# Kernel tuning notes

Hardware: AMD Instinct MI355X
Metric: run time of the kernel (lower is better)

## Reference

```python
import jax, jax.numpy as jnp
import numpy as np

N_HEAD = 16
NEG_INF = -1e9


def setup_inputs() -> dict:
    key = jax.random.key(0)
    k1, k2, k3 = jax.random.split(key, 3)
    B, S, D = 4, 1024, 1024
    x = jax.random.normal(k1, (B, S, D), dtype=jnp.float32)
    w_attn = jax.random.normal(k2, (D, 3 * D), dtype=jnp.float32) * 0.02
    b_attn = jnp.zeros((3 * D,), dtype=jnp.float32)
    w_proj = jax.random.normal(k3, (D, D), dtype=jnp.float32) * 0.02
    b_proj = jnp.zeros((D,), dtype=jnp.float32)
    return {"x": x, "w_attn": w_attn, "b_attn": b_attn,
            "w_proj": w_proj, "b_proj": b_proj}


def reference(x, w_attn, b_attn, w_proj, b_proj):
    B, S, D = x.shape
    H = N_HEAD
    hd = D // H
    # fused QKV Conv1D: addmm over flattened tokens
    qkv = x @ w_attn + b_attn                      # [B,S,3D]
    q, k, v = jnp.split(qkv, 3, axis=-1)           # each [B,S,D]
    # split heads -> [B,H,S,hd]
    def heads(t):
        return t.reshape(B, S, H, hd).transpose(0, 2, 1, 3)
    q, k, v = heads(q), heads(k), heads(v)
    # scaled dot-product with causal mask
    scores = jnp.einsum('bhqd,bhkd->bhqk', q, k) / jnp.sqrt(jnp.float32(hd))
    causal = jnp.tril(jnp.ones((S, S), dtype=bool))[None, None]  # [1,1,S,S]
    scores = jnp.where(causal, scores, NEG_INF)
    attn = jax.nn.softmax(scores, axis=-1)
    out = jnp.einsum('bhqk,bhkd->bhqd', attn, v)   # [B,H,S,hd]
    out = out.transpose(0, 2, 1, 3).reshape(B, S, D)  # merge heads
    # output projection Conv1D
    return out @ w_proj + b_proj
```

## Files before the change

### kernel.cpp

```cpp
#include <hip/hip_runtime.h>
#include <hip/hip_bf16.h>

typedef __attribute__((ext_vector_type(8))) __bf16 bf16x8;
typedef __attribute__((ext_vector_type(4))) float f32x4;

__device__ __forceinline__ unsigned short f2bf(float f) {
  unsigned int u = __builtin_bit_cast(unsigned int, f);
  u += 0x7fffu + ((u >> 16) & 1u);
  return (unsigned short)(u >> 16);
}

__device__ __forceinline__ unsigned int cvtpk_bf16(float a, float b) {
  unsigned int r;
  asm("v_cvt_pk_bf16_f32 %0, %1, %2" : "=v"(r) : "v"(a), "v"(b));
  return r;
}

__device__ __forceinline__ void gll16(const void* g, void* l) {
  __builtin_amdgcn_global_load_lds(
      (const __attribute__((address_space(1))) void*)g,
      (__attribute__((address_space(3))) void*)l, 16, 0, 0);
}

__device__ __forceinline__ bf16x8 lds_frag(const unsigned short* base, int row, int kbyte) {
  int off = row * 128 + (kbyte ^ ((row & 7) << 4));
  return *(const bf16x8*)((const char*)base + off);
}

#define QUAD(AF, BV, MO)                                                       \
  asm volatile("s_waitcnt lgkmcnt(0)" ::: "memory");                           \
  __builtin_amdgcn_sched_barrier(0);                                           \
  __builtin_amdgcn_s_setprio(1);                                               \
  _Pragma("unroll") for (int j = 0; j < 4; ++j)                                \
      _Pragma("unroll") for (int ni = 0; ni < 4; ++ni)                         \
          acc[MO + j][ni] = __builtin_amdgcn_mfma_f32_16x16x32_bf16(           \
              AF[j], BV[ni], acc[MO + j][ni], 0, 0, 0);                        \
  __builtin_amdgcn_s_setprio(0);                                               \
  __builtin_amdgcn_sched_barrier(0);

__global__ __launch_bounds__(256) void prep(
    const float* __restrict__ x, unsigned short* __restrict__ xb,
    const float* __restrict__ wa, unsigned short* __restrict__ waT,
    const float* __restrict__ wp, unsigned short* __restrict__ wpT) {
  __shared__ float tile[32][33];
  const int b = blockIdx.x;
  const int t = threadIdx.x;
  if (b < 4096) {
    int i = (b * 256 + t) * 4;
    float4 v = *(const float4*)(x + i);
    ushort4 o;
    o.x = f2bf(v.x); o.y = f2bf(v.y); o.z = f2bf(v.z); o.w = f2bf(v.w);
    *(ushort4*)(xb + i) = o;
    return;
  }
  const float* in;
  unsigned short* out;
  int bid, N;
  if (b < 7168) { in = wa; out = waT; bid = b - 4096; N = 3072; }
  else          { in = wp; out = wpT; bid = b - 7168; N = 1024; }
  const int K = 1024;
  int nb = N >> 5;
  int bx = bid % nb, by = bid / nb;
  int n0 = bx << 5, k0 = by << 5;
  int c = t & 31, r0 = t >> 5;
#pragma unroll
  for (int i = 0; i < 4; ++i) {
    int r = r0 + i * 8;
    tile[r][c] = in[(size_t)(k0 + r) * N + n0 + c];
  }
  __syncthreads();
#pragma unroll
  for (int i = 0; i < 4; ++i) {
    int r = r0 + i * 8;
    out[(size_t)(n0 + r) * K + k0 + c] = f2bf(tile[c][r]);
  }
}

__global__ __launch_bounds__(512, 2) void gemm_qkv256(
    const unsigned short* __restrict__ A, const unsigned short* __restrict__ Bt,
    const float* __restrict__ bias,
    unsigned short* __restrict__ Qg, unsigned short* __restrict__ Kg,
    unsigned short* __restrict__ Vtg, int K) {
  __shared__ __align__(16) unsigned short SMEM[65536];
  unsigned short* const A0 = SMEM;
  unsigned short* const B0 = SMEM + 16384;
  unsigned short* const A1 = SMEM + 32768;
  unsigned short* const B1 = SMEM + 49152;
  const int t = threadIdx.x;
  const int l = t & 63, lr = l & 15, hi = l >> 4;
  const int w = t >> 6;
  const int wr = w >> 2, wc = w & 3;
  const int bid = (int)(blockIdx.x % 8) * 24 + (int)(blockIdx.x / 8);
  const int bm = bid / 12, bn = bid % 12;
  const int m0 = bm << 8, n0 = bn << 8;
  const int wbase = (t & ~63) * 8;

  f32x4 acc[8][4] = {};

  auto stage_half = [&](int kt, int h, unsigned short* Ad, unsigned short* Bd) {
    const unsigned short* src;
    unsigned short* dst;
    if (h < 2) { src = A  + (size_t)(m0 + h * 128) * K + kt * 64;       dst = Ad + h * 8192; }
    else       { src = Bt + (size_t)(n0 + (h - 2) * 128) * K + kt * 64; dst = Bd + (h - 2) * 8192; }
#pragma unroll
    for (int i = 0; i < 2; ++i) {
      int ci = i * 512 + t;
      int row = ci >> 3, cpos = ci & 7;
      int c = cpos ^ (row & 7);
      gll16(src + (size_t)row * K + c * 8, dst + i * 4096 + wbase);
    }
  };

  auto lda = [&](bf16x8* af, const unsigned short* Ac, int mo, int kb) {
#pragma unroll
    for (int j = 0; j < 4; ++j)
      af[j] = lds_frag(Ac, wr * 128 + (mo + j) * 16 + lr, kb + hi * 16);
  };
  auto ldb = [&](bf16x8* bv, const unsigned short* Bc, int kb) {
#pragma unroll
    for (int j = 0; j < 4; ++j)
      bv[j] = lds_frag(Bc, wc * 64 + j * 16 + lr, kb + hi * 16);
  };

  const int nt = K >> 6;
  stage_half(0, 0, A0, B0); stage_half(0, 1, A0, B0);
  stage_half(0, 2, A0, B0); stage_half(0, 3, A0, B0);

  for (int T = 0; T < nt; ++T) {
    const unsigned short* Ac = (T & 1) ? A1 : A0;
    const unsigned short* Bc = (T & 1) ? B1 : B0;
    unsigned short* An = (T & 1) ? A0 : A1;
    unsigned short* Bn = (T & 1) ? B0 : B1;
    const bool pf = (T + 1 < nt);

    if (pf) {
      stage_half(T + 1, 0, An, Bn);
      asm volatile("s_waitcnt vmcnt(2)" ::: "memory");
    } else {
      asm volatile("s_waitcnt vmcnt(0)" ::: "memory");
    }
    __builtin_amdgcn_s_barrier();

    bf16x8 af[4], bv[4];
    ldb(bv, Bc, 0);
    lda(af, Ac, 0, 0);
    if (pf) stage_half(T + 1, 1, An, Bn);
    __builtin_amdgcn_s_barrier();
    QUAD(af, bv, 0);
    __builtin_amdgcn_s_barrier();
    lda(af, Ac, 4, 0);
    if (pf) stage_half(T + 1, 2, An, Bn);
    __builtin_amdgcn_s_barrier();
    QUAD(af, bv, 4);
    __builtin_amdgcn_s_barrier();
    ldb(bv, Bc, 64);
    lda(af, Ac, 0, 64);
    if (pf) stage_half(T + 1, 3, An, Bn);
    __builtin_amdgcn_s_barrier();
    QUAD(af, bv, 0);
    __builtin_amdgcn_s_barrier();
    lda(af, Ac, 4, 64);
    __builtin_amdgcn_s_barrier();
    QUAD(af, bv, 4);
    __builtin_amdgcn_s_barrier();
  }

  if (n0 < 2048) {
    const float QSCALE = 0.125f * 1.4426950408889634f;
#pragma unroll
    for (int mi = 0; mi < 8; ++mi)
#pragma unroll
      for (int ni = 0; ni < 4; ++ni)
#pragma unroll
        for (int r = 0; r < 4; ++r) {
          int m = m0 + wr * 128 + mi * 16 + 4 * hi + r;
          int n = n0 + wc * 64 + ni * 16 + lr;
          float v = acc[mi][ni][r] + bias[n];
          int b = m >> 10, s = m & 1023;
          int d = n & 1023;
          int h = d >> 6, di = d & 63;
          int bh = (b << 4) + h;
          if (n < 1024) Qg[((size_t)(bh << 10) + s) * 64 + di] = f2bf(v * QSCALE);
          else          Kg[((size_t)(bh << 10) + s) * 64 + di] = f2bf(v);
        }
  } else {
    __syncthreads();
#pragma unroll
    for (int mi = 0; mi < 8; ++mi)
#pragma unroll
      for (int ni = 0; ni < 4; ++ni) {
        int nl = wc * 64 + ni * 16 + lr;
        int ml = wr * 128 + mi * 16 + 4 * hi;
        ushort4 pk;
        pk.x = f2bf(acc[mi][ni][0] + bias[n0 + nl]);
        pk.y = f2bf(acc[mi][ni][1] + bias[n0 + nl]);
        pk.z = f2bf(acc[mi][ni][2] + bias[n0 + nl]);
        pk.w = f2bf(acc[mi][ni][3] + bias[n0 + nl]);
        *(ushort4*)&SMEM[nl * 256 + (ml ^ ((nl & 7) << 3))] = pk;
      }
    __syncthreads();
    const int b = m0 >> 10;
    const int sbase = m0 & 1023;
#pragma unroll
    for (int it = 0; it < 16; ++it) {
      int nl = it * 16 + (t >> 5);
      int s0 = (t & 31) * 8;
      bf16x8 v8 = *(const bf16x8*)&SMEM[nl * 256 + (s0 ^ ((nl & 7) << 3))];
      int d = n0 - 2048 + nl;
      size_t row = ((size_t)((b << 4) + (d >> 6)) << 6) + (d & 63);
      *(bf16x8*)&Vtg[row * 1024 + sbase + s0] = v8;
    }
  }
}

__global__ __launch_bounds__(256, 2) void gemm_proj128(
    const unsigned short* __restrict__ A, const unsigned short* __restrict__ Bt,
    const float* __restrict__ bias, float* __restrict__ outf,
    int M, int N, int K) {
  __shared__ unsigned short A0[128 * 64], B0[128 * 64];
  __shared__ unsigned short A1[128 * 64], B1[128 * 64];
  const int t = threadIdx.x;
  const int w = t >> 6, l = t & 63, lr = l & 15, hi = l >> 4;
  const int wr = w >> 1, wc = w & 1;
  const int nbn = N >> 7;
  const int nwg = (M >> 7) * nbn;
  int bid = (int)blockIdx.x;
  if ((nwg & 7) == 0) bid = (bid % 8) * (nwg / 8) + bid / 8;
  const int bm = bid / nbn, bn = bid % nbn;
  const int m0 = bm << 7, n0 = bn << 7;
  const int wbase = (t & ~63) * 8;

  f32x4 acc[4][4] = {};

  auto stage_half = [&](int kt, int h, unsigned short* Ad, unsigned short* Bd) {
    const unsigned short* src;
    unsigned short* dst;
    if (h < 2) { src = A  + (size_t)(m0 + h * 64) * K + kt * 64;       dst = Ad + h * 4096; }
    else       { src = Bt + (size_t)(n0 + (h - 2) * 64) * K + kt * 64; dst = Bd + (h - 2) * 4096; }
#pragma unroll
    for (int i = 0; i < 2; ++i) {
      int ci = i * 256 + t;
      int row = ci >> 3, cpos = ci & 7;
      int c = cpos ^ (row & 7);
      gll16(src + (size_t)row * K + c * 8, dst + i * 2048 + wbase);
    }
  };

  auto lda = [&](bf16x8* af, const unsigned short* Ac, int kb) {
#pragma unroll
    for (int j = 0; j < 4; ++j)
      af[j] = lds_frag(Ac, wr * 64 + j * 16 + lr, kb + hi * 16);
  };
  auto ldb = [&](bf16x8* bv, const unsigned short* Bc, int kb) {
#pragma unroll
    for (int j = 0; j < 4; ++j)
      bv[j] = lds_frag(Bc, wc * 64 + j * 16 + lr, kb + hi * 16);
  };

  const int nt = K >> 6;
  stage_half(0, 0, A0, B0); stage_half(0, 1, A0, B0);
  stage_half(0, 2, A0, B0); stage_half(0, 3, A0, B0);

  for (int T = 0; T < nt; ++T) {
    const unsigned short* Ac = (T & 1) ? A1 : A0;
    const unsigned short* Bc = (T & 1) ? B1 : B0;
    unsigned short* An = (T & 1) ? A0 : A1;
    unsigned short* Bn = (T & 1) ? B0 : B1;
    const bool pf = (T + 1 < nt);

    if (pf) {
      stage_half(T + 1, 0, An, Bn);
      asm volatile("s_waitcnt vmcnt(2)" ::: "memory");
    } else {
      asm volatile("s_waitcnt vmcnt(0)" ::: "memory");
    }
    __builtin_amdgcn_s_barrier();

    bf16x8 af[4], bv[4];
    ldb(bv, Bc, 0);
    lda(af, Ac, 0);
    if (pf) { stage_half(T + 1, 2, An, Bn); stage_half(T + 1, 1, An, Bn); }
    __builtin_amdgcn_s_barrier();
    QUAD(af, bv, 0);
    __builtin_amdgcn_s_barrier();
    ldb(bv, Bc, 64);
    lda(af, Ac, 64);
    if (pf) stage_half(T + 1, 3, An, Bn);
    __builtin_amdgcn_s_barrier();
    QUAD(af, bv, 0);
    __builtin_amdgcn_s_barrier();
  }

#pragma unroll
  for (int mi = 0; mi < 4; ++mi)
#pragma unroll
    for (int ni = 0; ni < 4; ++ni)
#pragma unroll
      for (int r = 0; r < 4; ++r) {
        int m = m0 + wr * 64 + mi * 16 + 4 * hi + r;
        int n = n0 + wc * 64 + ni * 16 + lr;
        outf[(size_t)m * N + n] = acc[mi][ni][r] + bias[n];
      }
}

__global__ __launch_bounds__(256) void attn_kernel(
    const unsigned short* __restrict__ Qg, const unsigned short* __restrict__ Kg,
    const unsigned short* __restrict__ Vtg, unsigned short* __restrict__ Og) {
  __shared__ unsigned short K0[64 * 64], K1[64 * 64];
  __shared__ unsigned short Vb[64 * 64];
  __shared__ __align__(16) unsigned short Plds[4][16][72];
  const int bh = blockIdx.x & 63;
  const int qt = blockIdx.x >> 6;
  const int t = threadIdx.x;
  const int w = t >> 6, l = t & 63, lr = l & 15, hi = l >> 4;
  const unsigned short* Qbh = Qg + (size_t)bh * 65536;
  const unsigned short* Kbh = Kg + (size_t)bh * 65536;
  const unsigned short* Vbh = Vtg + (size_t)bh * 65536;
  const int q0 = qt * 64 + w * 16;
  const int wbase = (t & ~63) * 8;

  bf16x8 qf[2];
#pragma unroll
  for (int ks = 0; ks < 2; ++ks)
    qf[ks] = *(const bf16x8*)(Qbh + (size_t)(q0 + lr) * 64 + ks * 32 + hi * 8);

  f32x4 ocT[4] = {};
  float mrun = -1e30f, lrun = 0.f;
  const int thr = w * 16 + lr - 4 * hi;

  auto stageK = [&](int kt, unsigned short* Kd) {
#pragma unroll
    for (int i = 0; i < 2; ++i) {
      int ci = i * 256 + t;
      int row = ci >> 3, cpos = ci & 7;
      int c = cpos ^ (row & 7);
      gll16(Kbh + (size_t)(kt * 64 + row) * 64 + c * 8, Kd + i * 2048 + wbase);
    }
  };
  auto stageV = [&](int kt) {
#pragma unroll
    for (int i = 0; i < 2; ++i) {
      int ci = i * 256 + t;
      int row = ci >> 3, cpos = ci & 7;
      int c = cpos ^ (row & 7);
      gll16(Vbh + (size_t)row * 1024 + kt * 64 + c * 8, Vb + i * 2048 + wbase);
    }
  };

  stageK(0, K0);
  stageV(0);

  for (int kt = 0; kt <= qt; ++kt) {
    unsigned short* Kc = (kt & 1) ? K1 : K0;
    unsigned short* Kn = (kt & 1) ? K0 : K1;
    const bool pf = (kt < qt);

    asm volatile("s_waitcnt vmcnt(2)" ::: "memory");
    __builtin_amdgcn_s_barrier();

    if (pf) stageK(kt + 1, Kn);

    f32x4 sc[4] = {};
    __builtin_amdgcn_s_setprio(1);
#pragma unroll
    for (int c = 0; c < 4; ++c)
#pragma unroll
      for (int ks = 0; ks < 2; ++ks) {
        bf16x8 kf = lds_frag(Kc, c * 16 + lr, ks * 64 + hi * 16);
        sc[c] = __builtin_amdgcn_mfma_f32_16x16x32_bf16(kf, qf[ks], sc[c], 0, 0, 0);
      }
    __builtin_amdgcn_s_setprio(0);
    if (kt == qt) {
#pragma unroll
      for (int c = 0; c < 4; ++c)
#pragma unroll
        for (int r = 0; r < 4; ++r)
          if (c * 16 + r > thr) sc[c][r] = -1e30f;
    }

    float mx = sc[0][0];
#pragma unroll
    for (int c = 0; c < 4; ++c)
#pragma unroll
      for (int r = 0; r < 4; ++r) mx = fmaxf(mx, sc[c][r]);
    mx = fmaxf(mx, __shfl_xor(mx, 16));
    mx = fmaxf(mx, __shfl_xor(mx, 32));
    if (!__all(mx <= mrun)) {
      float mn = fmaxf(mrun, mx);
      float al = exp2f(mrun - mn);
      mrun = mn;
      lrun *= al;
#pragma unroll
      for (int c = 0; c < 4; ++c)
#pragma unroll
        for (int r = 0; r < 4; ++r) ocT[c][r] *= al;
    }
    float p[4][4], s = 0.f;
#pragma unroll
    for (int c = 0; c < 4; ++c)
#pragma unroll
      for (int r = 0; r < 4; ++r) {
        p[c][r] = exp2f(sc[c][r] - mrun);
        s += p[c][r];
      }
    s += __shfl_xor(s, 16);
    s += __shfl_xor(s, 32);
    lrun += s;

#pragma unroll
    for (int c = 0; c < 4; ++c) {
      uint2 pk;
      pk.x = cvtpk_bf16(p[c][0], p[c][1]);
      pk.y = cvtpk_bf16(p[c][2], p[c][3]);
      *(uint2*)&Plds[w][lr][c * 16 + 4 * hi] = pk;
    }
    asm volatile("s_waitcnt lgkmcnt(0)" ::: "memory");
    __builtin_amdgcn_sched_barrier(0);

    bf16x8 pb[2];
#pragma unroll
    for (int ks = 0; ks < 2; ++ks)
      pb[ks] = *(const bf16x8*)(&Plds[w][lr][ks * 32 + hi * 8]);

    if (pf) asm volatile("s_waitcnt vmcnt(2)" ::: "memory");
    else    asm volatile("s_waitcnt vmcnt(0)" ::: "memory");
    __builtin_amdgcn_s_barrier();

    __builtin_amdgcn_s_setprio(1);
#pragma unroll
    for (int c = 0; c < 4; ++c)
#pragma unroll
      for (int ks = 0; ks < 2; ++ks) {
        bf16x8 vf = lds_frag(Vb, c * 16 + lr, ks * 64 + hi * 16);
        ocT[c] = __builtin_amdgcn_mfma_f32_16x16x32_bf16(vf, pb[ks], ocT[c], 0, 0, 0);
      }
    __builtin_amdgcn_s_setprio(0);
    __builtin_amdgcn_s_barrier();
    if (pf) stageV(kt + 1);
  }

  const int b = bh >> 4, h = bh & 15;
  const float inv = 1.0f / lrun;
  const size_t rowbase = ((size_t)(b * 1024 + q0 + lr)) * 1024 + h * 64;
#pragma unroll
  for (int c = 0; c < 4; ++c) {
    uint2 o2;
    o2.x = cvtpk_bf16(ocT[c][0] * inv, ocT[c][1] * inv);
    o2.y = cvtpk_bf16(ocT[c][2] * inv, ocT[c][3] * inv);
    *(uint2*)&Og[rowbase + c * 16 + 4 * hi] = o2;
  }
}

extern "C" void kernel_launch(void* const* d_in, const int* in_sizes, int n_in,
                              void* d_out, int out_size, void* d_ws, size_t ws_size,
                              hipStream_t stream) {
  const float* x      = (const float*)d_in[0];
  const float* w_attn = (const float*)d_in[1];
  const float* b_attn = (const float*)d_in[2];
  const float* w_proj = (const float*)d_in[3];
  const float* b_proj = (const float*)d_in[4];
  float* out = (float*)d_out;

  unsigned short* ws  = (unsigned short*)d_ws;
  unsigned short* xb  = ws;
  unsigned short* waT = xb + 4096 * 1024;
  unsigned short* wpT = waT + 3072 * 1024;
  unsigned short* Qg  = wpT + 1024 * 1024;
  unsigned short* Kg  = Qg + 4194304;
  unsigned short* Vtg = Kg + 4194304;
  unsigned short* Og  = xb;

  prep<<<8192, 256, 0, stream>>>(x, xb, w_attn, waT, w_proj, wpT);
  gemm_qkv256<<<16 * 12, 512, 0, stream>>>(xb, waT, b_attn, Qg, Kg, Vtg, 1024);
  attn_kernel<<<1024, 256, 0, stream>>>(Qg, Kg, Vtg, Og);
  gemm_proj128<<<32 * 8, 256, 0, stream>>>(Og, wpT, b_proj, (float*)out, 4096, 1024, 1024);
}
```

Measured before the change: 100.3 us.

## Drop LDS K/V staging in attention; give each wave an independent query tile

The attention kernel no longer stages K and V tiles into shared memory with double buffering and block barriers. Each wave now loads its K and V MFMA fragments straight from global memory into registers. The blocks' four waves are decoupled so each handles its own 16-row query tile and loops only up to its own causal limit, which reduces causal imbalance. The cost is that K/V reuse across the waves of a block is lost, global/L2 traffic goes up, and register pressure rises, with a launch bound of 4 blocks per SIMD now requested.

```diff
diff --git a/kernel.cpp b/kernel.cpp
--- a/kernel.cpp
+++ b/kernel.cpp
@@ -303,21 +303,19 @@
       }
 }
 
-__global__ __launch_bounds__(256) void attn_kernel(
+__global__ __launch_bounds__(256, 4) void attn_kernel(
     const unsigned short* __restrict__ Qg, const unsigned short* __restrict__ Kg,
     const unsigned short* __restrict__ Vtg, unsigned short* __restrict__ Og) {
-  __shared__ unsigned short K0[64 * 64], K1[64 * 64];
-  __shared__ unsigned short Vb[64 * 64];
   __shared__ __align__(16) unsigned short Plds[4][16][72];
-  const int bh = blockIdx.x & 63;
-  const int qt = blockIdx.x >> 6;
   const int t = threadIdx.x;
   const int w = t >> 6, l = t & 63, lr = l & 15, hi = l >> 4;
+  const int tid = (int)blockIdx.x * 4 + w;
+  const int bh = tid & 63;
+  const int qt16 = tid >> 6;
+  const int q0 = qt16 * 16;
   const unsigned short* Qbh = Qg + (size_t)bh * 65536;
   const unsigned short* Kbh = Kg + (size_t)bh * 65536;
   const unsigned short* Vbh = Vtg + (size_t)bh * 65536;
-  const int q0 = qt * 64 + w * 16;
-  const int wbase = (t & ~63) * 8;
 
   bf16x8 qf[2];
 #pragma unroll
@@ -326,51 +324,30 @@
 
   f32x4 ocT[4] = {};
   float mrun = -1e30f, lrun = 0.f;
-  const int thr = w * 16 + lr - 4 * hi;
-
-  auto stageK = [&](int kt, unsigned short* Kd) {
-#pragma unroll
-    for (int i = 0; i < 2; ++i) {
-      int ci = i * 256 + t;
-      int row = ci >> 3, cpos = ci & 7;
-      int c = cpos ^ (row & 7);
-      gll16(Kbh + (size_t)(kt * 64 + row) * 64 + c * 8, Kd + i * 2048 + wbase);
-    }
-  };
-  auto stageV = [&](int kt) {
-#pragma unroll
-    for (int i = 0; i < 2; ++i) {
-      int ci = i * 256 + t;
-      int row = ci >> 3, cpos = ci & 7;
-      int c = cpos ^ (row & 7);
-      gll16(Vbh + (size_t)row * 1024 + kt * 64 + c * 8, Vb + i * 2048 + wbase);
-    }
-  };
-
-  stageK(0, K0);
-  stageV(0);
-
-  for (int kt = 0; kt <= qt; ++kt) {
-    unsigned short* Kc = (kt & 1) ? K1 : K0;
-    unsigned short* Kn = (kt & 1) ? K0 : K1;
-    const bool pf = (kt < qt);
-
-    asm volatile("s_waitcnt vmcnt(2)" ::: "memory");
-    __builtin_amdgcn_s_barrier();
-
-    if (pf) stageK(kt + 1, Kn);
+  const int ktlast = qt16 >> 2;
+  const int thr = (qt16 & 3) * 16 + lr - 4 * hi;
+
+  const unsigned short* Krow = Kbh + lr * 64 + hi * 8;
+  const unsigned short* Vrow = Vbh + lr * 1024 + hi * 8;
+
+  for (int kt = 0; kt <= ktlast; ++kt) {
+    bf16x8 kf[4][2];
+#pragma unroll
+    for (int c = 0; c < 4; ++c)
+#pragma unroll
+      for (int ks = 0; ks < 2; ++ks)
+        kf[c][ks] = *(const bf16x8*)(Krow + kt * 4096 + c * 1024 + ks * 32);
 
     f32x4 sc[4] = {};
     __builtin_amdgcn_s_setprio(1);
 #pragma unroll
     for (int c = 0; c < 4; ++c)
 #pragma unroll
-      for (int ks = 0; ks < 2; ++ks) {
-        bf16x8 kf = lds_frag(Kc, c * 16 + lr, ks * 64 + hi * 16);
-        sc[c] = __builtin_amdgcn_mfma_f32_16x16x32_bf16(kf, qf[ks], sc[c], 0, 0, 0);
-      }
+      for (int ks = 0; ks < 2; ++ks)
+        sc[c] = __builtin_amdgcn_mfma_f32_16x16x32_bf16(kf[c][ks], qf[ks], sc[c], 0, 0, 0);
     __builtin_amdgcn_s_setprio(0);
-    if (kt == qt) {
+
+    if (kt == ktlast) {
 #pragma unroll
       for (int c = 0; c < 4; ++c)
 #pragma unroll
@@ -422,21 +399,19 @@
     for (int ks = 0; ks < 2; ++ks)
       pb[ks] = *(const bf16x8*)(&Plds[w][lr][ks * 32 + hi * 8]);
 
-    if (pf) asm volatile("s_waitcnt vmcnt(2)" ::: "memory");
-    else    asm volatile("s_waitcnt vmcnt(0)" ::: "memory");
-    __builtin_amdgcn_s_barrier();
-
+    bf16x8 vf[4][2];
+#pragma unroll
+    for (int c = 0; c < 4; ++c)
+#pragma unroll
+      for (int ks = 0; ks < 2; ++ks)
+        vf[c][ks] = *(const bf16x8*)(Vrow + c * 16384 + kt * 64 + ks * 32);
     __builtin_amdgcn_s_setprio(1);
 #pragma unroll
     for (int c = 0; c < 4; ++c)
 #pragma unroll
-      for (int ks = 0; ks < 2; ++ks) {
-        bf16x8 vf = lds_frag(Vb, c * 16 + lr, ks * 64 + hi * 16);
-        ocT[c] = __builtin_amdgcn_mfma_f32_16x16x32_bf16(vf, pb[ks], ocT[c], 0, 0, 0);
-      }
+      for (int ks = 0; ks < 2; ++ks)
+        ocT[c] = __builtin_amdgcn_mfma_f32_16x16x32_bf16(vf[c][ks], pb[ks], ocT[c], 0, 0, 0);
     __builtin_amdgcn_s_setprio(0);
-    __builtin_amdgcn_s_barrier();
-    if (pf) stageV(kt + 1);
   }
 
   const int b = bh >> 4, h = bh & 15;
```

New measurement: 140.9 us. 1.4x slower.

## Replace fine-grained interleaved GEMM pipeline with simple double-buffered stage/compute loop

Applied to the files above, without the earlier changes.

Both bf16 GEMM kernels (QKV and output projection) drop the hand-interleaved schedule, which split each K-tile's global-to-LDS loads into quarters with explicit vmcnt waits and many s_barriers between MFMA groups. They now issue the whole next tile's loads up front, run all MFMAs for the current tile, and end with a single __syncthreads. This removes most barriers and lets the compiler schedule LDS reads and MFMAs freely. In exchange it gives up the explicit control over overlap of loads, LDS reads and MFMAs, and holds more fragment registers at once (8 A fragments in the QKV kernel).

```diff
diff --git a/kernel.cpp b/kernel.cpp
--- a/kernel.cpp
+++ b/kernel.cpp
@@ -26,17 +26,6 @@
   int off = row * 128 + (kbyte ^ ((row & 7) << 4));
   return *(const bf16x8*)((const char*)base + off);
 }
-
-#define QUAD(AF, BV, MO)                                                       \
-  asm volatile("s_waitcnt lgkmcnt(0)" ::: "memory");                           \
-  __builtin_amdgcn_sched_barrier(0);                                           \
-  __builtin_amdgcn_s_setprio(1);                                               \
-  _Pragma("unroll") for (int j = 0; j < 4; ++j)                                \
-      _Pragma("unroll") for (int ni = 0; ni < 4; ++ni)                         \
-          acc[MO + j][ni] = __builtin_amdgcn_mfma_f32_16x16x32_bf16(           \
-              AF[j], BV[ni], acc[MO + j][ni], 0, 0, 0);                        \
-  __builtin_amdgcn_s_setprio(0);                                               \
-  __builtin_amdgcn_sched_barrier(0);
 
 __global__ __launch_bounds__(256) void prep(
     const float* __restrict__ x, unsigned short* __restrict__ xb,
@@ -97,72 +86,46 @@
 
   f32x4 acc[8][4] = {};
 
-  auto stage_half = [&](int kt, int h, unsigned short* Ad, unsigned short* Bd) {
-    const unsigned short* src;
-    unsigned short* dst;
-    if (h < 2) { src = A  + (size_t)(m0 + h * 128) * K + kt * 64;       dst = Ad + h * 8192; }
-    else       { src = Bt + (size_t)(n0 + (h - 2) * 128) * K + kt * 64; dst = Bd + (h - 2) * 8192; }
-#pragma unroll
-    for (int i = 0; i < 2; ++i) {
+  auto stage = [&](int kt, unsigned short* Ad, unsigned short* Bd) {
+    const unsigned short* Ab = A + (size_t)m0 * K + kt * 64;
+    const unsigned short* Bb = Bt + (size_t)n0 * K + kt * 64;
+#pragma unroll
+    for (int i = 0; i < 4; ++i) {
       int ci = i * 512 + t;
       int row = ci >> 3, cpos = ci & 7;
       int c = cpos ^ (row & 7);
-      gll16(src + (size_t)row * K + c * 8, dst + i * 4096 + wbase);
-    }
-  };
-
-  auto lda = [&](bf16x8* af, const unsigned short* Ac, int mo, int kb) {
-#pragma unroll
-    for (int j = 0; j < 4; ++j)
-      af[j] = lds_frag(Ac, wr * 128 + (mo + j) * 16 + lr, kb + hi * 16);
-  };
-  auto ldb = [&](bf16x8* bv, const unsigned short* Bc, int kb) {
-#pragma unroll
-    for (int j = 0; j < 4; ++j)
-      bv[j] = lds_frag(Bc, wc * 64 + j * 16 + lr, kb + hi * 16);
+      gll16(Ab + (size_t)row * K + c * 8, Ad + i * 4096 + wbase);
+      gll16(Bb + (size_t)row * K + c * 8, Bd + i * 4096 + wbase);
+    }
+  };
+
+  auto compute = [&](const unsigned short* Ad, const unsigned short* Bd) {
+#pragma unroll
+    for (int ks = 0; ks < 2; ++ks) {
+      bf16x8 af[8], bv[4];
+#pragma unroll
+      for (int mi = 0; mi < 8; ++mi)
+        af[mi] = lds_frag(Ad, wr * 128 + mi * 16 + lr, ks * 64 + hi * 16);
+#pragma unroll
+      for (int ni = 0; ni < 4; ++ni)
+        bv[ni] = lds_frag(Bd, wc * 64 + ni * 16 + lr, ks * 64 + hi * 16);
+      __builtin_amdgcn_s_setprio(1);
+#pragma unroll
+      for (int mi = 0; mi < 8; ++mi)
+#pragma unroll
+        for (int ni = 0; ni < 4; ++ni)
+          acc[mi][ni] = __builtin_amdgcn_mfma_f32_16x16x32_bf16(af[mi], bv[ni], acc[mi][ni], 0, 0, 0);
+      __builtin_amdgcn_s_setprio(0);
+    }
   };
 
   const int nt = K >> 6;
-  stage_half(0, 0, A0, B0); stage_half(0, 1, A0, B0);
-  stage_half(0, 2, A0, B0); stage_half(0, 3, A0, B0);
-
+  stage(0, A0, B0);
+  __syncthreads();
   for (int T = 0; T < nt; ++T) {
-    const unsigned short* Ac = (T & 1) ? A1 : A0;
-    const unsigned short* Bc = (T & 1) ? B1 : B0;
-    unsigned short* An = (T & 1) ? A0 : A1;
-    unsigned short* Bn = (T & 1) ? B0 : B1;
-    const bool pf = (T + 1 < nt);
-
-    if (pf) {
-      stage_half(T + 1, 0, An, Bn);
-      asm volatile("s_waitcnt vmcnt(2)" ::: "memory");
-    } else {
-      asm volatile("s_waitcnt vmcnt(0)" ::: "memory");
-    }
-    __builtin_amdgcn_s_barrier();
-
-    bf16x8 af[4], bv[4];
-    ldb(bv, Bc, 0);
-    lda(af, Ac, 0, 0);
-    if (pf) stage_half(T + 1, 1, An, Bn);
-    __builtin_amdgcn_s_barrier();
-    QUAD(af, bv, 0);
-    __builtin_amdgcn_s_barrier();
-    lda(af, Ac, 4, 0);
-    if (pf) stage_half(T + 1, 2, An, Bn);
-    __builtin_amdgcn_s_barrier();
-    QUAD(af, bv, 4);
-    __builtin_amdgcn_s_barrier();
-    ldb(bv, Bc, 64);
-    lda(af, Ac, 0, 64);
-    if (pf) stage_half(T + 1, 3, An, Bn);
-    __builtin_amdgcn_s_barrier();
-    QUAD(af, bv, 0);
-    __builtin_amdgcn_s_barrier();
-    lda(af, Ac, 4, 64);
-    __builtin_amdgcn_s_barrier();
-    QUAD(af, bv, 4);
-    __builtin_amdgcn_s_barrier();
+    if (T + 1 < nt) stage(T + 1, (T & 1) ? A0 : A1, (T & 1) ? B0 : B1);
+    compute((T & 1) ? A1 : A0, (T & 1) ? B1 : B0);
+    __syncthreads();
   }
 
   if (n0 < 2048) {
@@ -232,63 +195,46 @@
 
   f32x4 acc[4][4] = {};
 
-  auto stage_half = [&](int kt, int h, unsigned short* Ad, unsigned short* Bd) {
-    const unsigned short* src;
-    unsigned short* dst;
-    if (h < 2) { src = A  + (size_t)(m0 + h * 64) * K + kt * 64;       dst = Ad + h * 4096; }
-    else       { src = Bt + (size_t)(n0 + (h - 2) * 64) * K + kt * 64; dst = Bd + (h - 2) * 4096; }
-#pragma unroll
-    for (int i = 0; i < 2; ++i) {
+  auto stage = [&](int kt, unsigned short* Ad, unsigned short* Bd) {
+    const unsigned short* Ab = A + (size_t)m0 * K + kt * 64;
+    const unsigned short* Bb = Bt + (size_t)n0 * K + kt * 64;
+#pragma unroll
+    for (int i = 0; i < 4; ++i) {
       int ci = i * 256 + t;
       int row = ci >> 3, cpos = ci & 7;
       int c = cpos ^ (row & 7);
-      gll16(src + (size_t)row * K + c * 8, dst + i * 2048 + wbase);
-    }
-  };
-
-  auto lda = [&](bf16x8* af, const unsigned short* Ac, int kb) {
-#pragma unroll
-    for (int j = 0; j < 4; ++j)
-      af[j] = lds_frag(Ac, wr * 64 + j * 16 + lr, kb + hi * 16);
-  };
-  auto ldb = [&](bf16x8* bv, const unsigned short* Bc, int kb) {
-#pragma unroll
-    for (int j = 0; j < 4; ++j)
-      bv[j] = lds_frag(Bc, wc * 64 + j * 16 + lr, kb + hi * 16);
+      gll16(Ab + (size_t)row * K + c * 8, Ad + i * 2048 + wbase);
+      gll16(Bb + (size_t)row * K + c * 8, Bd + i * 2048 + wbase);
+    }
+  };
+
+  auto compute = [&](const unsigned short* Ad, const unsigned short* Bd) {
+#pragma unroll
+    for (int ks = 0; ks < 2; ++ks) {
+      bf16x8 af[4], bv[4];
+#pragma unroll
+      for (int mi = 0; mi < 4; ++mi)
+        af[mi] = lds_frag(Ad, wr * 64 + mi * 16 + lr, ks * 64 + hi * 16);
+#pragma unroll
+      for (int ni = 0; ni < 4; ++ni)
+        bv[ni] = lds_frag(Bd, wc * 64 + ni * 16 + lr, ks * 64 + hi * 16);
+      __builtin_amdgcn_s_setprio(1);
+#pragma unroll
+      for (int mi = 0; mi < 4; ++mi)
+#pragma unroll
+        for (int ni = 0; ni < 4; ++ni)
+          acc[mi][ni] = __builtin_amdgcn_mfma_f32_16x16x32_bf16(af[mi], bv[ni], acc[mi][ni], 0, 0, 0);
+      __builtin_amdgcn_s_setprio(0);
+    }
   };
 
   const int nt = K >> 6;
-  stage_half(0, 0, A0, B0); stage_half(0, 1, A0, B0);
-  stage_half(0, 2, A0, B0); stage_half(0, 3, A0, B0);
-
+  stage(0, A0, B0);
+  __syncthreads();
   for (int T = 0; T < nt; ++T) {
-    const unsigned short* Ac = (T & 1) ? A1 : A0;
-    const unsigned short* Bc = (T & 1) ? B1 : B0;
-    unsigned short* An = (T & 1) ? A0 : A1;
-    unsigned short* Bn = (T & 1) ? B0 : B1;
-    const bool pf = (T + 1 < nt);
-
-    if (pf) {
-      stage_half(T + 1, 0, An, Bn);
-      asm volatile("s_waitcnt vmcnt(2)" ::: "memory");
-    } else {
-      asm volatile("s_waitcnt vmcnt(0)" ::: "memory");
-    }
-    __builtin_amdgcn_s_barrier();
-
-    bf16x8 af[4], bv[4];
-    ldb(bv, Bc, 0);
-    lda(af, Ac, 0);
-    if (pf) { stage_half(T + 1, 2, An, Bn); stage_half(T + 1, 1, An, Bn); }
-    __builtin_amdgcn_s_barrier();
-    QUAD(af, bv, 0);
-    __builtin_amdgcn_s_barrier();
-    ldb(bv, Bc, 64);
-    lda(af, Ac, 64);
-    if (pf) stage_half(T + 1, 3, An, Bn);
-    __builtin_amdgcn_s_barrier();
-    QUAD(af, bv, 0);
-    __builtin_amdgcn_s_barrier();
+    if (T + 1 < nt) stage(T + 1, (T & 1) ? A0 : A1, (T & 1) ? B0 : B1);
+    compute((T & 1) ? A1 : A0, (T & 1) ? B1 : B0);
+    __syncthreads();
   }
 
 #pragma unroll
```

New measurement: 97.59 us. -2.7%, faster.
